# Optimization experiments

Hardware: AMD Instinct MI355X
Metric: run time of the kernel (lower is better)

Reference implementation:

```python
import jax, jax.numpy as jnp
import numpy as np

N = 100000   # nodes
E = 1600000  # edges
F = 128      # in = hidden channels
L = 4        # num GCN layers
G = 512      # graphs in batch
OUT = 10     # classes
EPS = 1e-5


def setup_inputs() -> dict:
    key = jax.random.key(0)
    ks = jax.random.split(key, 12)
    x = jax.random.normal(ks[0], (N, F), dtype=jnp.float32)
    edge_index = jax.random.randint(ks[1], (2, E), 0, N, dtype=jnp.int64)
    batch = jnp.sort(jax.random.randint(ks[2], (N,), 0, G, dtype=jnp.int64))
    s = 1.0 / np.sqrt(F)
    Ws = jax.random.uniform(ks[3], (L, F, F), jnp.float32, -s, s)
    bs = jax.random.uniform(ks[4], (L, F), jnp.float32, -s, s)
    gammas = jnp.ones((L, F), jnp.float32)
    betas = jnp.zeros((L, F), jnp.float32)
    s1 = 1.0 / np.sqrt(F * L)
    W1 = jax.random.uniform(ks[5], (F * L, F), jnp.float32, -s1, s1)
    b1 = jax.random.uniform(ks[6], (F,), jnp.float32, -s1, s1)
    g1 = jnp.ones((F,), jnp.float32)
    bt1 = jnp.zeros((F,), jnp.float32)
    s2 = 1.0 / np.sqrt(F)
    W2 = jax.random.uniform(ks[7], (F, OUT), jnp.float32, -s2, s2)
    b2 = jax.random.uniform(ks[8], (OUT,), jnp.float32, -s2, s2)
    return {"x": x, "edge_index": edge_index, "batch": batch, "Ws": Ws, "bs": bs,
            "gammas": gammas, "betas": betas, "W1": W1, "b1": b1, "g1": g1,
            "bt1": bt1, "W2": W2, "b2": b2}


def _batch_norm(x, g, b):
    # training-mode BatchNorm1d over the node dim (biased variance)
    mu = jnp.mean(x, axis=0)
    var = jnp.var(x, axis=0)
    return (x - mu) * jax.lax.rsqrt(var + EPS) * g + b


def reference(x, edge_index, batch, Ws, bs, gammas, betas, W1, b1, g1, bt1, W2, b2):
    row, col = edge_index[0], edge_index[1]
    # GCN normalization (add_self_loops=False since normalize=True)
    deg = jax.ops.segment_sum(jnp.ones((E,), x.dtype), col, num_segments=N)
    dinv = jnp.where(deg > 0, jax.lax.rsqrt(deg), 0.0)
    norm = dinv[row] * dinv[col]  # [E]
    pooled = []
    h = x
    for t in range(L):
        hw = h @ Ws[t]                                    # [N, F]
        msg = norm[:, None] * hw[row]                     # gather  [E, F]
        h = jax.ops.segment_sum(msg, col, num_segments=N) + bs[t]  # scatter [N, F]
        h = jax.nn.relu(h)
        h = _batch_norm(h, gammas[t], betas[t])
        pooled.append(jax.ops.segment_sum(h, batch, num_segments=G))  # [G, F]
    z = jnp.concatenate(pooled, axis=1)                   # [G, L*F]
    z = z @ W1 + b1
    z = _batch_norm(z, g1, bt1)
    z = jax.nn.relu(z)
    return z @ W2 + b2                                    # [G, OUT]
```

## Files before the change

### kernel.cpp

```cpp
#include <hip/hip_runtime.h>

#define NN 100000
#define EE 1600000
#define FF 128
#define LL 4
#define GG 512
#define OUTC 10
#define EPSF 1e-5f
#define NSCB ((NN + 255) / 256)

#define NPW 16
#define AGG_WAVES ((NN + NPW - 1) / NPW)
#define AGG_BLOCKS ((AGG_WAVES + 3) / 4)

typedef __attribute__((ext_vector_type(8))) short short8;
typedef __attribute__((ext_vector_type(4))) float f32x4;

__device__ inline unsigned bf16rne(float f) {
  unsigned u = __float_as_uint(f);
  return (u + 0x7fffu + ((u >> 16) & 1u)) >> 16;
}
__device__ inline unsigned packbf(float lo, float hi) {
  return bf16rne(lo) | (bf16rne(hi) << 16);
}
__device__ inline float bflo(unsigned u) { return __uint_as_float(u << 16); }
__device__ inline float bfhi(unsigned u) { return __uint_as_float(u & 0xffff0000u); }


__global__ __launch_bounds__(256) void k_deg(const int* __restrict__ col, int* __restrict__ deg) {
  int e = blockIdx.x * 256 + threadIdx.x;
  if (e < EE) atomicAdd(&deg[col[e]], 1);
}

__global__ __launch_bounds__(256) void k_dinv(const int* __restrict__ deg, float* __restrict__ dinv) {
  int n = blockIdx.x * 256 + threadIdx.x;
  if (n < NN) {
    int d = deg[n];
    dinv[n] = d > 0 ? rsqrtf((float)d) : 0.0f;
  }
}

__global__ __launch_bounds__(256) void k_bsum(const int* __restrict__ deg, int* __restrict__ bsum) {
  int i = blockIdx.x * 256 + threadIdx.x;
  int v = (i < NN) ? deg[i] : 0;
#pragma unroll
  for (int off = 32; off > 0; off >>= 1) v += __shfl_down(v, off, 64);
  __shared__ int ws[4];
  if ((threadIdx.x & 63) == 0) ws[threadIdx.x >> 6] = v;
  __syncthreads();
  if (threadIdx.x == 0) bsum[blockIdx.x] = ws[0] + ws[1] + ws[2] + ws[3];
}

__global__ __launch_bounds__(256) void k_rowptr(const int* __restrict__ deg,
                                                const int* __restrict__ bsum,
                                                int* __restrict__ rowptr) {
  __shared__ int sb[512];
  __shared__ int sd[256];
  const int t = threadIdx.x;
  sb[t]       = (t < NSCB) ? bsum[t] : 0;
  sb[t + 256] = (t + 256 < NSCB) ? bsum[t + 256] : 0;
  __syncthreads();
#pragma unroll
  for (int off = 1; off < 512; off <<= 1) {
    int v0 = (t >= off) ? sb[t - off] : 0;
    int v1 = sb[t + 256 - off];
    __syncthreads();
    sb[t] += v0;
    sb[t + 256] += v1;
    __syncthreads();
  }
  const int bpre = (blockIdx.x == 0) ? 0 : sb[blockIdx.x - 1];
  const int i = blockIdx.x * 256 + t;
  const int d = (i < NN) ? deg[i] : 0;
  sd[t] = d;
  __syncthreads();
#pragma unroll
  for (int off = 1; off < 256; off <<= 1) {
    int v = (t >= off) ? sd[t - off] : 0;
    __syncthreads();
    sd[t] += v;
    __syncthreads();
  }
  if (i < NN) rowptr[i] = bpre + sd[t] - d;
  if (blockIdx.x == 0 && t == 0) rowptr[NN] = EE;
}

__global__ __launch_bounds__(256) void k_fill(const int* __restrict__ ei,
                                              const int* __restrict__ rowptr,
                                              int* __restrict__ cnt,
                                              const float* __restrict__ dinv,
                                              int2* __restrict__ ecw) {
  int e = blockIdx.x * 256 + threadIdx.x;
  if (e >= EE) return;
  int r = ei[e];
  int cl = ei[EE + e];
  int slot = rowptr[cl] + atomicAdd(&cnt[cl], 1);
  ecw[slot] = make_int2(r, __float_as_int(dinv[r] * dinv[cl]));
}

__global__ __launch_bounds__(256) void k_bounds(const int* __restrict__ batch, int* __restrict__ gstart) {
  int n = blockIdx.x * 256 + threadIdx.x;
  if (n >= NN) return;
  int b = batch[n];
  if (n == 0) {
    for (int g = 0; g <= b; ++g) gstart[g] = 0;
  } else {
    int bp = batch[n - 1];
    for (int g = bp + 1; g <= b; ++g) gstart[g] = n;
  }
  if (n == NN - 1) {
    for (int g = b + 1; g <= GG; ++g) gstart[g] = NN;
  }
}


__global__ __launch_bounds__(256) void k_cvt(const float* __restrict__ x, unsigned* __restrict__ Ab) {
  int i = blockIdx.x * 256 + threadIdx.x;
  if (i < NN * 64) {
    float2 v = *(const float2*)(x + (size_t)i * 2);
    Ab[i] = packbf(v.x, v.y);
  }
}

__global__ __launch_bounds__(256) void k_wcvt(const float* __restrict__ Ws, uint4* __restrict__ Wf) {
  int tid = blockIdx.x * 256 + threadIdx.x;
  int t = tid >> 12;
  int r = tid & 4095;
  int lane = r & 63;
  int which = (r >> 6) & 1;
  int ct = (r >> 7) & 7;
  int kc = r >> 10;
  int n = ct * 16 + (lane & 15);
  int k0 = kc * 32 + (lane >> 4) * 8;
  const float* W = Ws + t * 16384;
  unsigned h[8];
#pragma unroll
  for (int j = 0; j < 8; ++j) {
    float w = W[(k0 + j) * 128 + n];
    unsigned hb = bf16rne(w);
    if (which == 0) {
      h[j] = hb;
    } else {
      float hf = __uint_as_float(hb << 16);
      h[j] = bf16rne(w - hf);
    }
  }
  uint4 o;
  o.x = h[0] | (h[1] << 16);
  o.y = h[2] | (h[3] << 16);
  o.z = h[4] | (h[5] << 16);
  o.w = h[6] | (h[7] << 16);
  Wf[tid] = o;
}

__global__ __launch_bounds__(256) void k_mm(const unsigned* __restrict__ Ab,
                                            const uint4* __restrict__ Wf,
                                            unsigned* __restrict__ Bb) {
  const int lane = threadIdx.x & 63;
  const int w = threadIdx.x >> 6;
  const int quad = lane >> 4;
  const int m = lane & 15;
  const int rowbase = blockIdx.x * 64 + w * 16;
  const int arow = min(rowbase + m, NN - 1);
  const uint4* A4 = (const uint4*)Ab;
  f32x4 acc[8];
#pragma unroll
  for (int ct = 0; ct < 8; ++ct) acc[ct] = (f32x4){0.f, 0.f, 0.f, 0.f};
#pragma unroll
  for (int kc = 0; kc < 4; ++kc) {
    uint4 av = A4[arow * 16 + kc * 4 + quad];
    short8 af = *(short8*)&av;
#pragma unroll
    for (int ct = 0; ct < 8; ++ct) {
      uint4 bh = Wf[((kc * 8 + ct) * 2 + 0) * 64 + lane];
      uint4 bl = Wf[((kc * 8 + ct) * 2 + 1) * 64 + lane];
      acc[ct] = __builtin_amdgcn_mfma_f32_16x16x32_bf16(af, *(short8*)&bh, acc[ct], 0, 0, 0);
      acc[ct] = __builtin_amdgcn_mfma_f32_16x16x32_bf16(af, *(short8*)&bl, acc[ct], 0, 0, 0);
    }
  }
#pragma unroll
  for (int ct = 0; ct < 8; ++ct) {
#pragma unroll
    for (int r = 0; r < 4; ++r) {
      float v = acc[ct][r];
      float vo = __shfl_xor(v, 1);
      int row = rowbase + quad * 4 + r;
      if ((lane & 1) == 0 && row < NN) {
        Bb[row * 64 + ct * 8 + (m >> 1)] = packbf(v, vo);
      }
    }
  }
}

__global__ __launch_bounds__(256) void k_agg(const unsigned* __restrict__ Bb,
                                             const int* __restrict__ rowptr,
                                             const int2* __restrict__ ecw,
                                             const float* __restrict__ bias,
                                             unsigned* __restrict__ Ar,
                                             float* __restrict__ bnbuf) {
  const int lane = threadIdx.x & 63;
  const int wave = threadIdx.x >> 6;
  const int c = lane * 2;
  const int gwave = blockIdx.x * 4 + wave;
  const int n0 = gwave * NPW;
  const float2 bv = *(const float2*)(bias + c);
  float s0 = 0.f, s1 = 0.f, q0 = 0.f, q1 = 0.f;
  __shared__ int srp[4][NPW + 1];
  __shared__ int2 sstage[4][64];
  if (n0 < NN) {
    const int nn = min(NPW, NN - n0);
    if (lane <= nn) srp[wave][lane] = rowptr[n0 + lane];
    float ax0 = 0.f, ax1 = 0.f, ay0 = 0.f, ay1 = 0.f;
    auto finalize = [&](int node) {
      float rx = fmaxf(ax0 + ax1 + bv.x, 0.f);
      float ry = fmaxf(ay0 + ay1 + bv.y, 0.f);
      Ar[(size_t)(n0 + node) * 64 + lane] = packbf(rx, ry);
      s0 += rx; s1 += ry;
      q0 = fmaf(rx, rx, q0); q1 = fmaf(ry, ry, q1);
      ax0 = 0.f; ax1 = 0.f; ay0 = 0.f; ay1 = 0.f;
    };
    const int beg = __builtin_amdgcn_readfirstlane(srp[wave][0]);
    const int endall = __builtin_amdgcn_readfirstlane(srp[wave][nn]);
    int cn = 0;
    while (cn < nn && __builtin_amdgcn_readfirstlane(srp[wave][cn + 1]) == beg) {
      finalize(cn);
      ++cn;
    }
    int nend = (cn < nn) ? __builtin_amdgcn_readfirstlane(srp[wave][cn + 1]) : 0x7fffffff;
    int2 stage = (beg + lane < endall) ? ecw[beg + lane] : make_int2(0, 0);
    for (int base = beg; base < endall; base += 64) {
      sstage[wave][lane] = stage;
      const int nb = base + 64;
      if (nb < endall) {
        stage = (nb + lane < endall) ? ecw[nb + lane] : make_int2(0, 0);
      }
#pragma unroll
      for (int g = 0; g < 4; ++g) {
        if (base + g * 16 < endall) {
          int2 ew[16]; unsigned us[16];
#pragma unroll
          for (int j = 0; j < 16; ++j) ew[j] = sstage[wave][g * 16 + j];
#pragma unroll
          for (int j = 0; j < 16; ++j) {
            const int sj = __builtin_amdgcn_readfirstlane(ew[j].x);
            us[j] = Bb[((size_t)(unsigned)sj << 6) + (unsigned)lane];
          }
#pragma unroll
          for (int j = 0; j < 16; ++j) {
            const float wj = __int_as_float(ew[j].y);
            if (j & 1) {
              ax1 = fmaf(wj, bflo(us[j]), ax1);
              ay1 = fmaf(wj, bfhi(us[j]), ay1);
            } else {
              ax0 = fmaf(wj, bflo(us[j]), ax0);
              ay0 = fmaf(wj, bfhi(us[j]), ay0);
            }
            const int e1 = base + g * 16 + j + 1;
            if (e1 == nend) {
              finalize(cn);
              ++cn;
              nend = (cn < nn) ? __builtin_amdgcn_readfirstlane(srp[wave][cn + 1]) : 0x7fffffff;
              while (cn < nn && nend == e1) {
                finalize(cn);
                ++cn;
                nend = (cn < nn) ? __builtin_amdgcn_readfirstlane(srp[wave][cn + 1]) : 0x7fffffff;
              }
            }
          }
        }
      }
    }
  }
  __shared__ float sred[4][256];
  sred[wave][c] = s0;
  sred[wave][c + 1] = s1;
  sred[wave][128 + c] = q0;
  sred[wave][128 + c + 1] = q1;
  __syncthreads();
  const int t = threadIdx.x;
  float tot = sred[0][t] + sred[1][t] + sred[2][t] + sred[3][t];
  atomicAdd(&bnbuf[t], tot);
}

__global__ __launch_bounds__(128) void k_bnfin(const float* __restrict__ bnbuf,
                                               const float* __restrict__ gamma,
                                               const float* __restrict__ beta,
                                               float* __restrict__ bnsc) {
  const int c = threadIdx.x;
  float mu = bnbuf[c] * (1.0f / NN);
  float var = bnbuf[128 + c] * (1.0f / NN) - mu * mu;
  float inv = rsqrtf(var + EPSF);
  float sc = gamma[c] * inv;
  bnsc[c] = sc;
  bnsc[128 + c] = beta[c] - mu * sc;
}

__global__ __launch_bounds__(128) void k_bnapply(const unsigned* __restrict__ Ar,
                                                 const float* __restrict__ bnsc,
                                                 const int* __restrict__ gstart,
                                                 float* __restrict__ pooledt,
                                                 unsigned* __restrict__ Ab) {
  const int g = blockIdx.x >> 3;
  const int sub = blockIdx.x & 7;
  const int s = gstart[g];
  const int e = gstart[g + 1];
  const int cnt = e - s;
  if (cnt <= 0) return;
  const int per = (cnt + 7) >> 3;
  const int ns = s + sub * per;
  const int ne = min(ns + per, e);
  if (ns >= ne) return;
  const int cp = threadIdx.x & 63;
  const int half = threadIdx.x >> 6;
  const float2 sc = *(const float2*)(bnsc + 2 * cp);
  const float2 sh = *(const float2*)(bnsc + 128 + 2 * cp);
  float accx = 0.f, accy = 0.f;
  for (int n = ns + half; n < ne; n += 2) {
    unsigned u = Ar[(size_t)n * 64 + cp];
    float vx = fmaf(bflo(u), sc.x, sh.x);
    float vy = fmaf(bfhi(u), sc.y, sh.y);
    Ab[(size_t)n * 64 + cp] = packbf(vx, vy);
    accx += vx;
    accy += vy;
  }
  atomicAdd(&pooledt[(size_t)g * 512 + 2 * cp], accx);
  atomicAdd(&pooledt[(size_t)g * 512 + 2 * cp + 1], accy);
}


__global__ __launch_bounds__(128) void k_z1(const float* __restrict__ pooled,
                                            const float* __restrict__ W1,
                                            const float* __restrict__ b1,
                                            float* __restrict__ z1) {
  __shared__ float sp[512];
  const int g = blockIdx.x;
  for (int i = threadIdx.x; i < 512; i += 128) sp[i] = pooled[(size_t)g * 512 + i];
  __syncthreads();
  const int c = threadIdx.x;
  float acc = b1[c];
  for (int j = 0; j < 512; ++j) acc = fmaf(sp[j], W1[j * 128 + c], acc);
  z1[(size_t)g * 128 + c] = acc;
}

__global__ __launch_bounds__(128) void k_zstat(const float* __restrict__ z1,
                                               const float* __restrict__ g1,
                                               const float* __restrict__ bt1,
                                               float* __restrict__ zsc) {
  const int c = threadIdx.x;
  float s = 0.f, q = 0.f;
  for (int g = 0; g < GG; ++g) {
    float v = z1[g * 128 + c];
    s += v;
    q = fmaf(v, v, q);
  }
  float mu = s * (1.0f / GG);
  float var = q * (1.0f / GG) - mu * mu;
  float inv = rsqrtf(var + EPSF);
  float sc = g1[c] * inv;
  zsc[c] = sc;
  zsc[128 + c] = bt1[c] - mu * sc;
}

__global__ __launch_bounds__(128) void k_out(const float* __restrict__ z1,
                                             const float* __restrict__ zsc,
                                             const float* __restrict__ W2,
                                             const float* __restrict__ b2,
                                             float* __restrict__ out) {
  __shared__ float zr[128];
  const int g = blockIdx.x;
  const int c = threadIdx.x;
  zr[c] = fmaxf(fmaf(z1[(size_t)g * 128 + c], zsc[c], zsc[128 + c]), 0.f);
  __syncthreads();
  if (c < OUTC) {
    float acc = b2[c];
    for (int k = 0; k < 128; ++k) acc = fmaf(zr[k], W2[k * OUTC + c], acc);
    out[(size_t)g * OUTC + c] = acc;
  }
}


extern "C" void kernel_launch(void* const* d_in, const int* in_sizes, int n_in,
                              void* d_out, int out_size, void* d_ws, size_t ws_size,
                              hipStream_t stream) {
  const float* x      = (const float*)d_in[0];
  const int*   ei     = (const int*)d_in[1];
  const int*   batch  = (const int*)d_in[2];
  const float* Ws     = (const float*)d_in[3];
  const float* bs     = (const float*)d_in[4];
  const float* gammas = (const float*)d_in[5];
  const float* betas  = (const float*)d_in[6];
  const float* W1     = (const float*)d_in[7];
  const float* b1     = (const float*)d_in[8];
  const float* g1     = (const float*)d_in[9];
  const float* bt1    = (const float*)d_in[10];
  const float* W2     = (const float*)d_in[11];
  const float* b2     = (const float*)d_in[12];
  float* out = (float*)d_out;

  char* ws = (char*)d_ws;
  size_t off = 0;
  auto alloc = [&](size_t bytes) -> void* {
    void* p = ws + off;
    off = (off + bytes + 255) & ~(size_t)255;
    return p;
  };
  int*   deg    = (int*)alloc((size_t)NN * 4);
  int*   cnt    = (int*)alloc((size_t)NN * 4);
  float* bnbuf  = (float*)alloc((size_t)LL * 256 * 4);
  float* pooled = (float*)alloc((size_t)GG * 512 * 4);
  size_t zero_bytes = off;
  unsigned* Ar     = (unsigned*)alloc((size_t)NN * 64 * 4);
  unsigned* Ab     = (unsigned*)alloc((size_t)NN * 64 * 4);
  unsigned* Bb     = (unsigned*)alloc((size_t)NN * 64 * 4);
  int2*     ecw    = (int2*)alloc((size_t)EE * 8);
  float*    dinv   = (float*)alloc((size_t)NN * 4);
  int*      rowptr = (int*)alloc((size_t)(NN + 1) * 4);
  int*      bsum   = (int*)alloc((size_t)NSCB * 4);
  int*      gstart = (int*)alloc((size_t)(GG + 1) * 4);
  uint4*    Wf     = (uint4*)alloc((size_t)LL * 4096 * 16);
  float*    z1     = (float*)alloc((size_t)GG * FF * 4);
  float*    bnsc   = (float*)alloc(256 * 4);
  float*    zsc    = (float*)alloc(256 * 4);
  (void)ws_size; (void)in_sizes; (void)n_in; (void)out_size;

  hipMemsetAsync(d_ws, 0, zero_bytes, stream);

  k_deg<<<(EE + 255) / 256, 256, 0, stream>>>(ei + EE, deg);
  k_dinv<<<(NN + 255) / 256, 256, 0, stream>>>(deg, dinv);
  k_bsum<<<NSCB, 256, 0, stream>>>(deg, bsum);
  k_rowptr<<<NSCB, 256, 0, stream>>>(deg, bsum, rowptr);
  k_fill<<<(EE + 255) / 256, 256, 0, stream>>>(ei, rowptr, cnt, dinv, ecw);
  k_bounds<<<(NN + 255) / 256, 256, 0, stream>>>(batch, gstart);
  k_cvt<<<(NN * 64 + 255) / 256, 256, 0, stream>>>(x, Ab);
  k_wcvt<<<64, 256, 0, stream>>>(Ws, Wf);

  for (int t = 0; t < LL; ++t) {
    k_mm<<<(NN + 63) / 64, 256, 0, stream>>>(Ab, Wf + (size_t)t * 4096, Bb);
    k_agg<<<AGG_BLOCKS, 256, 0, stream>>>(Bb, rowptr, ecw, bs + t * FF, Ar, bnbuf + t * 256);
    k_bnfin<<<1, 128, 0, stream>>>(bnbuf + t * 256, gammas + t * FF, betas + t * FF, bnsc);
    k_bnapply<<<GG * 8, 128, 0, stream>>>(Ar, bnsc, gstart, pooled + t * FF, Ab);
  }

  k_z1<<<GG, 128, 0, stream>>>(pooled, W1, b1, z1);
  k_zstat<<<1, 128, 0, stream>>>(z1, g1, bt1, zsc);
  k_out<<<GG, 128, 0, stream>>>(z1, zsc, W2, b2, out);
}
```

Measured before the change: 840.4 us.

## Fold BatchNorm affine into next layer weights and pool inside aggregation

Removes the separate BN-apply pass by folding the per-channel BN scale into the next layer's weight matrix and the BN shift into a per-node term (shift·W scaled by the node's summed edge weight) added during aggregation. Pooling of the raw ReLU outputs moves into the aggregation kernel through per-graph atomics, and BN is applied to the pooled sums afterwards in k_z1 using node counts. It also halves nodes per wave in aggregation and adds an occupancy hint. The cost is extra atomics for the edge-weight sums and the pooling, plus small per-layer weight-conversion kernels.

```diff
diff --git a/kernel.cpp b/kernel.cpp
--- a/kernel.cpp
+++ b/kernel.cpp
@@ -9,7 +9,7 @@
 #define EPSF 1e-5f
 #define NSCB ((NN + 255) / 256)
 
-#define NPW 16
+#define NPW 8
 #define AGG_WAVES ((NN + NPW - 1) / NPW)
 #define AGG_BLOCKS ((AGG_WAVES + 3) / 4)
 
@@ -89,13 +89,16 @@
                                               const int* __restrict__ rowptr,
                                               int* __restrict__ cnt,
                                               const float* __restrict__ dinv,
-                                              int2* __restrict__ ecw) {
+                                              int2* __restrict__ ecw,
+                                              float* __restrict__ swsum) {
   int e = blockIdx.x * 256 + threadIdx.x;
   if (e >= EE) return;
   int r = ei[e];
   int cl = ei[EE + e];
+  float w = dinv[r] * dinv[cl];
   int slot = rowptr[cl] + atomicAdd(&cnt[cl], 1);
-  ecw[slot] = make_int2(r, __float_as_int(dinv[r] * dinv[cl]));
+  ecw[slot] = make_int2(r, __float_as_int(w));
+  atomicAdd(&swsum[cl], w);
 }
 
 __global__ __launch_bounds__(256) void k_bounds(const int* __restrict__ batch, int* __restrict__ gstart) {
@@ -122,21 +125,21 @@
   }
 }
 
-__global__ __launch_bounds__(256) void k_wcvt(const float* __restrict__ Ws, uint4* __restrict__ Wf) {
+__global__ __launch_bounds__(256) void k_wcvt(const float* __restrict__ W,
+                                              const float* __restrict__ sc,
+                                              uint4* __restrict__ Wf) {
   int tid = blockIdx.x * 256 + threadIdx.x;
-  int t = tid >> 12;
-  int r = tid & 4095;
-  int lane = r & 63;
-  int which = (r >> 6) & 1;
-  int ct = (r >> 7) & 7;
-  int kc = r >> 10;
+  int lane = tid & 63;
+  int which = (tid >> 6) & 1;
+  int ct = (tid >> 7) & 7;
+  int kc = tid >> 10;
   int n = ct * 16 + (lane & 15);
   int k0 = kc * 32 + (lane >> 4) * 8;
-  const float* W = Ws + t * 16384;
   unsigned h[8];
 #pragma unroll
   for (int j = 0; j < 8; ++j) {
     float w = W[(k0 + j) * 128 + n];
+    if (sc) w *= sc[k0 + j];
     unsigned hb = bf16rne(w);
     if (which == 0) {
       h[j] = hb;
@@ -151,6 +154,15 @@
   o.z = h[4] | (h[5] << 16);
   o.w = h[6] | (h[7] << 16);
   Wf[tid] = o;
+}
+
+__global__ __launch_bounds__(128) void k_base(const float* __restrict__ W,
+                                              const float* __restrict__ bnsc,
+                                              float* __restrict__ base) {
+  const int c = threadIdx.x;
+  float acc = 0.f;
+  for (int k = 0; k < 128; ++k) acc = fmaf(bnsc[128 + k], W[k * 128 + c], acc);
+  base[c] = acc;
 }
 
 __global__ __launch_bounds__(256) void k_mm(const unsigned* __restrict__ Ab,
@@ -192,31 +204,50 @@
   }
 }
 
-__global__ __launch_bounds__(256) void k_agg(const unsigned* __restrict__ Bb,
-                                             const int* __restrict__ rowptr,
-                                             const int2* __restrict__ ecw,
-                                             const float* __restrict__ bias,
-                                             unsigned* __restrict__ Ar,
-                                             float* __restrict__ bnbuf) {
+__global__ __launch_bounds__(256, 8) void k_agg(const unsigned* __restrict__ Bb,
+                                                const int* __restrict__ rowptr,
+                                                const int2* __restrict__ ecw,
+                                                const float* __restrict__ bias,
+                                                const float* __restrict__ base,
+                                                const float* __restrict__ swsum,
+                                                const int* __restrict__ batch,
+                                                unsigned* __restrict__ Ar,
+                                                float* __restrict__ bnbuf,
+                                                float* __restrict__ pooledt) {
   const int lane = threadIdx.x & 63;
   const int wave = threadIdx.x >> 6;
   const int c = lane * 2;
   const int gwave = blockIdx.x * 4 + wave;
   const int n0 = gwave * NPW;
   const float2 bv = *(const float2*)(bias + c);
+  const float2 basev = *(const float2*)(base + c);
   float s0 = 0.f, s1 = 0.f, q0 = 0.f, q1 = 0.f;
   __shared__ int srp[4][NPW + 1];
   __shared__ int2 sstage[4][64];
   if (n0 < NN) {
     const int nn = min(NPW, NN - n0);
     if (lane <= nn) srp[wave][lane] = rowptr[n0 + lane];
+    int bsp = 0; float swp = 0.f;
+    if (lane < nn) { bsp = batch[n0 + lane]; swp = swsum[n0 + lane]; }
     float ax0 = 0.f, ax1 = 0.f, ay0 = 0.f, ay1 = 0.f;
+    float px = 0.f, py = 0.f;
+    int gprev = -1;
     auto finalize = [&](int node) {
-      float rx = fmaxf(ax0 + ax1 + bv.x, 0.f);
-      float ry = fmaxf(ay0 + ay1 + bv.y, 0.f);
+      float sw = __shfl(swp, node);
+      float rx = fmaxf(fmaf(sw, basev.x, ax0 + ax1) + bv.x, 0.f);
+      float ry = fmaxf(fmaf(sw, basev.y, ay0 + ay1) + bv.y, 0.f);
       Ar[(size_t)(n0 + node) * 64 + lane] = packbf(rx, ry);
       s0 += rx; s1 += ry;
       q0 = fmaf(rx, rx, q0); q1 = fmaf(ry, ry, q1);
+      int g = __shfl(bsp, node);
+      if (g != gprev) {
+        if (gprev >= 0) {
+          atomicAdd(&pooledt[(size_t)gprev * 512 + c], px);
+          atomicAdd(&pooledt[(size_t)gprev * 512 + c + 1], py);
+        }
+        gprev = g; px = 0.f; py = 0.f;
+      }
+      px += rx; py += ry;
       ax0 = 0.f; ax1 = 0.f; ay0 = 0.f; ay1 = 0.f;
     };
     const int beg = __builtin_amdgcn_readfirstlane(srp[wave][0]);
@@ -228,15 +259,15 @@
     }
     int nend = (cn < nn) ? __builtin_amdgcn_readfirstlane(srp[wave][cn + 1]) : 0x7fffffff;
     int2 stage = (beg + lane < endall) ? ecw[beg + lane] : make_int2(0, 0);
-    for (int base = beg; base < endall; base += 64) {
+    for (int base_e = beg; base_e < endall; base_e += 64) {
       sstage[wave][lane] = stage;
-      const int nb = base + 64;
+      const int nb = base_e + 64;
       if (nb < endall) {
         stage = (nb + lane < endall) ? ecw[nb + lane] : make_int2(0, 0);
       }
 #pragma unroll
       for (int g = 0; g < 4; ++g) {
-        if (base + g * 16 < endall) {
+        if (base_e + g * 16 < endall) {
           int2 ew[16]; unsigned us[16];
 #pragma unroll
           for (int j = 0; j < 16; ++j) ew[j] = sstage[wave][g * 16 + j];
@@ -255,7 +286,7 @@
               ax0 = fmaf(wj, bflo(us[j]), ax0);
               ay0 = fmaf(wj, bfhi(us[j]), ay0);
             }
-            const int e1 = base + g * 16 + j + 1;
+            const int e1 = base_e + g * 16 + j + 1;
             if (e1 == nend) {
               finalize(cn);
               ++cn;
@@ -270,6 +301,10 @@
         }
       }
     }
+    if (gprev >= 0) {
+      atomicAdd(&pooledt[(size_t)gprev * 512 + c], px);
+      atomicAdd(&pooledt[(size_t)gprev * 512 + c + 1], py);
+    }
   }
   __shared__ float sred[4][256];
   sred[wave][c] = s0;
@@ -295,46 +330,20 @@
   bnsc[128 + c] = beta[c] - mu * sc;
 }
 
-__global__ __launch_bounds__(128) void k_bnapply(const unsigned* __restrict__ Ar,
-                                                 const float* __restrict__ bnsc,
-                                                 const int* __restrict__ gstart,
-                                                 float* __restrict__ pooledt,
-                                                 unsigned* __restrict__ Ab) {
-  const int g = blockIdx.x >> 3;
-  const int sub = blockIdx.x & 7;
-  const int s = gstart[g];
-  const int e = gstart[g + 1];
-  const int cnt = e - s;
-  if (cnt <= 0) return;
-  const int per = (cnt + 7) >> 3;
-  const int ns = s + sub * per;
-  const int ne = min(ns + per, e);
-  if (ns >= ne) return;
-  const int cp = threadIdx.x & 63;
-  const int half = threadIdx.x >> 6;
-  const float2 sc = *(const float2*)(bnsc + 2 * cp);
-  const float2 sh = *(const float2*)(bnsc + 128 + 2 * cp);
-  float accx = 0.f, accy = 0.f;
-  for (int n = ns + half; n < ne; n += 2) {
-    unsigned u = Ar[(size_t)n * 64 + cp];
-    float vx = fmaf(bflo(u), sc.x, sh.x);
-    float vy = fmaf(bfhi(u), sc.y, sh.y);
-    Ab[(size_t)n * 64 + cp] = packbf(vx, vy);
-    accx += vx;
-    accy += vy;
-  }
-  atomicAdd(&pooledt[(size_t)g * 512 + 2 * cp], accx);
-  atomicAdd(&pooledt[(size_t)g * 512 + 2 * cp + 1], accy);
-}
-
-
-__global__ __launch_bounds__(128) void k_z1(const float* __restrict__ pooled,
+
+__global__ __launch_bounds__(128) void k_z1(const float* __restrict__ S,
+                                            const float* __restrict__ bnscL,
+                                            const int* __restrict__ gstart,
                                             const float* __restrict__ W1,
                                             const float* __restrict__ b1,
                                             float* __restrict__ z1) {
   __shared__ float sp[512];
   const int g = blockIdx.x;
-  for (int i = threadIdx.x; i < 512; i += 128) sp[i] = pooled[(size_t)g * 512 + i];
+  const float cntg = (float)(gstart[g + 1] - gstart[g]);
+  for (int i = threadIdx.x; i < 512; i += 128) {
+    int t = i >> 7, ch = i & 127;
+    sp[i] = fmaf(bnscL[t * 256 + ch], S[(size_t)g * 512 + i], cntg * bnscL[t * 256 + 128 + ch]);
+  }
   __syncthreads();
   const int c = threadIdx.x;
   float acc = b1[c];
@@ -408,6 +417,8 @@
   int*   cnt    = (int*)alloc((size_t)NN * 4);
   float* bnbuf  = (float*)alloc((size_t)LL * 256 * 4);
   float* pooled = (float*)alloc((size_t)GG * 512 * 4);
+  float* swsum  = (float*)alloc((size_t)NN * 4);
+  float* zbase  = (float*)alloc(128 * 4);
   size_t zero_bytes = off;
   unsigned* Ar     = (unsigned*)alloc((size_t)NN * 64 * 4);
   unsigned* Ab     = (unsigned*)alloc((size_t)NN * 64 * 4);
@@ -417,9 +428,10 @@
   int*      rowptr = (int*)alloc((size_t)(NN + 1) * 4);
   int*      bsum   = (int*)alloc((size_t)NSCB * 4);
   int*      gstart = (int*)alloc((size_t)(GG + 1) * 4);
-  uint4*    Wf     = (uint4*)alloc((size_t)LL * 4096 * 16);
+  uint4*    Wf     = (uint4*)alloc((size_t)4096 * 16);
   float*    z1     = (float*)alloc((size_t)GG * FF * 4);
-  float*    bnsc   = (float*)alloc(256 * 4);
+  float*    bnscL  = (float*)alloc((size_t)LL * 256 * 4);
+  float*    basebf = (float*)alloc(128 * 4);
   float*    zsc    = (float*)alloc(256 * 4);
   (void)ws_size; (void)in_sizes; (void)n_in; (void)out_size;
 
@@ -429,19 +441,25 @@
   k_dinv<<<(NN + 255) / 256, 256, 0, stream>>>(deg, dinv);
   k_bsum<<<NSCB, 256, 0, stream>>>(deg, bsum);
   k_rowptr<<<NSCB, 256, 0, stream>>>(deg, bsum, rowptr);
-  k_fill<<<(EE + 255) / 256, 256, 0, stream>>>(ei, rowptr, cnt, dinv, ecw);
+  k_fill<<<(EE + 255) / 256, 256, 0, stream>>>(ei, rowptr, cnt, dinv, ecw, swsum);
   k_bounds<<<(NN + 255) / 256, 256, 0, stream>>>(batch, gstart);
   k_cvt<<<(NN * 64 + 255) / 256, 256, 0, stream>>>(x, Ab);
-  k_wcvt<<<64, 256, 0, stream>>>(Ws, Wf);
+  k_wcvt<<<16, 256, 0, stream>>>(Ws, nullptr, Wf);
 
   for (int t = 0; t < LL; ++t) {
-    k_mm<<<(NN + 63) / 64, 256, 0, stream>>>(Ab, Wf + (size_t)t * 4096, Bb);
-    k_agg<<<AGG_BLOCKS, 256, 0, stream>>>(Bb, rowptr, ecw, bs + t * FF, Ar, bnbuf + t * 256);
-    k_bnfin<<<1, 128, 0, stream>>>(bnbuf + t * 256, gammas + t * FF, betas + t * FF, bnsc);
-    k_bnapply<<<GG * 8, 128, 0, stream>>>(Ar, bnsc, gstart, pooled + t * FF, Ab);
-  }
-
-  k_z1<<<GG, 128, 0, stream>>>(pooled, W1, b1, z1);
+    k_mm<<<(NN + 63) / 64, 256, 0, stream>>>(t == 0 ? Ab : Ar, Wf, Bb);
+    k_agg<<<AGG_BLOCKS, 256, 0, stream>>>(Bb, rowptr, ecw, bs + t * FF,
+                                          t == 0 ? zbase : basebf, swsum, batch,
+                                          Ar, bnbuf + t * 256, pooled + t * FF);
+    k_bnfin<<<1, 128, 0, stream>>>(bnbuf + t * 256, gammas + t * FF, betas + t * FF,
+                                   bnscL + t * 256);
+    if (t < LL - 1) {
+      k_wcvt<<<16, 256, 0, stream>>>(Ws + (size_t)(t + 1) * 16384, bnscL + t * 256, Wf);
+      k_base<<<1, 128, 0, stream>>>(Ws + (size_t)(t + 1) * 16384, bnscL + t * 256, basebf);
+    }
+  }
+
+  k_z1<<<GG, 128, 0, stream>>>(pooled, bnscL, gstart, W1, b1, z1);
   k_zstat<<<1, 128, 0, stream>>>(z1, g1, bt1, zsc);
   k_out<<<GG, 128, 0, stream>>>(z1, zsc, W2, b2, out);
 }
```

Result: slower. 1.897 ms (+125.8%).
